# Kernel tuning notes

Measured on AMD Instinct MI355X. Metric: run time of the kernel, lower is better.

## Reference

```python
import jax, jax.numpy as jnp
import numpy as np

B, OUT, EXC_IN, INH_IN, BF = 8192, 1024, 4096, 2048, 4
K_EXC, K_INH = 32, 16


def _pruned_weight(pre_w, K):
    # TopKLinear.pruned_weight: mask of top-K entries (by pre_w) times exp(pre_w)
    w = jnp.exp(pre_w)                      # param_space='log'
    _, idx = jax.lax.top_k(pre_w, K)        # [out, K] indices per row
    rows = jnp.arange(pre_w.shape[0])[:, None]
    mask = jnp.zeros_like(pre_w).at[rows, idx].set(1.0)
    return mask * w


def setup_inputs() -> dict:
    key = jax.random.key(0)
    ks = jax.random.split(key, 5)
    return {
        "x": jax.random.normal(ks[0], (B, EXC_IN), jnp.float32),
        "inhibitory_input": jax.random.normal(ks[1], (B, INH_IN), jnp.float32),
        "branch_input": jax.random.normal(ks[2], (B, OUT * BF), jnp.float32),
        "pre_w_exc": jax.random.uniform(ks[3], (OUT, EXC_IN), jnp.float32, -2.1, -2.0),
        "pre_w_inh": jax.random.uniform(ks[4], (OUT, INH_IN), jnp.float32, -2.1, -2.0),
        "w_block": jnp.ones((OUT, BF), jnp.float32),          # BlockLinear weight (init ones, frozen)
        "presigmoid_Vth": jnp.full((OUT,), -2.0, jnp.float32),  # uniform(-2,-2) == constant
        "log_alpha_max": jnp.zeros((OUT,), jnp.float32),
    }


def reference(x, inhibitory_input, branch_input, pre_w_exc, pre_w_inh,
              w_block, presigmoid_Vth, log_alpha_max):
    # TopKLinear forward: x @ pruned_weight.T
    excitation = x @ _pruned_weight(pre_w_exc, K_EXC).T            # [B, OUT]
    inhibition = inhibitory_input @ _pruned_weight(pre_w_inh, K_INH).T  # [B, OUT]

    # BlockLinear: scatter w_block into block-diagonal [OUT, OUT*BF] then mm;
    # equivalent contraction over the block dim only.
    current = jnp.einsum('nob,ob->no', branch_input.reshape(B, OUT, BF), w_block)
    conductance = jnp.sum(w_block, axis=1)                         # [OUT]

    numerator = excitation + current
    denominator = excitation + 1.0 + conductance + inhibition
    voltage = numerator / denominator

    # reactivation
    Vth = jax.nn.sigmoid(presigmoid_Vth)
    V_diff = voltage - Vth
    rate = jnp.exp(log_alpha_max) * V_diff * V_diff
    return jnp.where(V_diff < 0, jnp.zeros((), voltage.dtype), rate)
```

## Files before the change

### kernel.cpp

```cpp
#include <hip/hip_runtime.h>
#include <cstdint>
#include <cstddef>

#define B_ROWS 8192
#define OUT_N  1024
#define EXC_IN 4096
#define INH_IN 2048
#define K_EXC  32
#define K_INH  16

#define TILE_N       2
#define MAIN_THREADS 1024
#define NBLK         512
#define NT_PER_BLK   (B_ROWS / TILE_N / NBLK)
#define COMB_FLOATS  ((EXC_IN + INH_IN) * TILE_N)
#define CHUNKS       (COMB_FLOATS / 64)
#define CHUNKS_PER_WAVE (CHUNKS / (MAIN_THREADS / 64))
#define XCHUNKS      (EXC_IN * TILE_N / 64)

template<int COLS, int K>
__device__ __forceinline__ void topk_row(const float* __restrict__ src,
                                         float2* __restrict__ ocol, int lane)
{
    constexpr int E4 = COLS / 256;
    unsigned long long keys[E4 * 4];
#pragma unroll
    for (int i = 0; i < E4; ++i) {
        const float4 v = ((const float4*)src)[i * 64 + lane];
        const float vv[4] = {v.x, v.y, v.z, v.w};
#pragma unroll
        for (int q = 0; q < 4; ++q) {
            const int idx = (i * 64 + lane) * 4 + q;
            const unsigned int u = __float_as_uint(vv[q]);
            const unsigned int m = (u >> 31) ? ~u : (u | 0x80000000u);
            keys[i * 4 + q] = ((unsigned long long)m << 12)
                            | (unsigned long long)(4095 - idx);
        }
    }

    unsigned long long win = 0xFFFFFFFFFFFFFFFFull;
#pragma unroll 1
    for (int r = 0; r < K; ++r) {
        unsigned long long best = 0ull;
#pragma unroll
        for (int i = 0; i < E4 * 4; ++i) {
            const unsigned long long k2 = (keys[i] == win) ? 0ull : keys[i];
            keys[i] = k2;
            best = (k2 > best) ? k2 : best;
        }
#pragma unroll
        for (int m = 1; m < 64; m <<= 1) {
            const unsigned long long o = __shfl_xor(best, m, 64);
            best = (o > best) ? o : best;
        }
        win = best;
        if (lane == 0) {
            const unsigned int idx = 4095u - (unsigned int)(win & 0xFFFull);
            const unsigned int mm  = (unsigned int)(win >> 12);
            const unsigned int u   = (mm & 0x80000000u) ? (mm & 0x7FFFFFFFu) : ~mm;
            const float v = __uint_as_float(u);
            ocol[(size_t)r * OUT_N] = make_float2(expf(v), __uint_as_float(idx));
        }
    }
}

__global__ __launch_bounds__(256, 1) void topk_both_kernel(
    const float* __restrict__ pwe, const float* __restrict__ pwi,
    float2* __restrict__ wexcT, float2* __restrict__ winhT)
{
    const int wid  = (blockIdx.x * 256 + threadIdx.x) >> 6;
    const int lane = threadIdx.x & 63;
    if (wid < OUT_N) {
        topk_row<EXC_IN, K_EXC>(pwe + (size_t)wid * EXC_IN, wexcT + wid, lane);
    } else {
        const int r = wid - OUT_N;
        topk_row<INH_IN, K_INH>(pwi + (size_t)r * INH_IN, winhT + r, lane);
    }
}

typedef __attribute__((address_space(1))) const unsigned int gu32_t;
typedef __attribute__((address_space(3))) unsigned int lu32_t;

__global__ __launch_bounds__(MAIN_THREADS, 4) void dendritic_main_kernel(
    const float*  __restrict__ x,
    const float*  __restrict__ inh,
    const float4* __restrict__ branch,
    const float2* __restrict__ wexcT,
    const float2* __restrict__ winhT,
    const float4* __restrict__ wblock,
    const float*  __restrict__ presig,
    const float*  __restrict__ logalpha,
    float*        __restrict__ out)
{
    __shared__ float sx[2][COMB_FLOATS];

    const int tid  = threadIdx.x;
    const int lane = tid & 63;
    const int w    = tid >> 6;
    const int o    = tid;

    const float4 wb   = wblock[o];
    const float cond  = wb.x + wb.y + wb.z + wb.w;
    const float Vth   = 1.f / (1.f + expf(-presig[o]));
    const float alpha = expf(logalpha[o]);

    const int tile0 = blockIdx.x * NT_PER_BLK;
    const int srow  = lane & 1;
    const int scol  = lane >> 1;

    {
        const int n0 = tile0 * TILE_N;
        const float* xs = x   + (size_t)(n0 + srow) * EXC_IN + scol;
        const float* is = inh + (size_t)(n0 + srow) * INH_IN + scol;
#pragma unroll
        for (int i = 0; i < CHUNKS_PER_WAVE; ++i) {
            const int c = i * 16 + w;
            const float* src = (c < XCHUNKS) ? (xs + c * 32)
                                             : (is + (c - XCHUNKS) * 32);
            __builtin_amdgcn_global_load_lds((gu32_t*)src,
                                             (lu32_t*)(&sx[0][0] + c * 64),
                                             4, 0, 0);
        }
    }

#pragma unroll 1
    for (int t = 0; t < NT_PER_BLK; ++t) {
        const int n0 = (tile0 + t) * TILE_N;
        const float* buf = &sx[t & 1][0];

        if (t + 1 < NT_PER_BLK) {
            const int n1 = n0 + TILE_N;
            const float* xs = x   + (size_t)(n1 + srow) * EXC_IN + scol;
            const float* is = inh + (size_t)(n1 + srow) * INH_IN + scol;
            float* dst = &sx[(t + 1) & 1][0];
#pragma unroll
            for (int i = 0; i < CHUNKS_PER_WAVE; ++i) {
                const int c = i * 16 + w;
                const float* src = (c < XCHUNKS) ? (xs + c * 32)
                                                 : (is + (c - XCHUNKS) * 32);
                __builtin_amdgcn_global_load_lds((gu32_t*)src,
                                                 (lu32_t*)(dst + c * 64),
                                                 4, 0, 0);
            }
        }

        const float4 br0 = branch[(size_t)(n0 + 0) * OUT_N + o];
        const float4 br1 = branch[(size_t)(n0 + 1) * OUT_N + o];

        if (t + 1 < NT_PER_BLK) {
            asm volatile("s_waitcnt vmcnt(14)" ::: "memory");
        } else {
            asm volatile("s_waitcnt vmcnt(2)" ::: "memory");
        }
        __builtin_amdgcn_s_barrier();

        float e0 = 0.f, e1 = 0.f;
#pragma unroll 8
        for (int k = 0; k < K_EXC; ++k) {
            const float2 wv = wexcT[k * OUT_N + o];
            const int c = (int)__float_as_uint(wv.y);
            const float2 xv = ((const float2*)buf)[c];
            e0 = fmaf(xv.x, wv.x, e0);
            e1 = fmaf(xv.y, wv.x, e1);
        }

        float i0 = 0.f, i1 = 0.f;
#pragma unroll 8
        for (int k = 0; k < K_INH; ++k) {
            const float2 wv = winhT[k * OUT_N + o];
            const int c = (int)__float_as_uint(wv.y);
            const float2 xv = ((const float2*)buf)[EXC_IN + c];
            i0 = fmaf(xv.x, wv.x, i0);
            i1 = fmaf(xv.y, wv.x, i1);
        }

        {
            const float cur0 = br0.x * wb.x + br0.y * wb.y + br0.z * wb.z + br0.w * wb.w;
            const float cur1 = br1.x * wb.x + br1.y * wb.y + br1.z * wb.z + br1.w * wb.w;
            const float v0 = (e0 + cur0) / (e0 + 1.f + cond + i0);
            const float v1 = (e1 + cur1) / (e1 + 1.f + cond + i1);
            const float d0 = v0 - Vth;
            const float d1 = v1 - Vth;
            const float r0 = alpha * d0 * d0;
            const float r1 = alpha * d1 * d1;
            out[(size_t)(n0 + 0) * OUT_N + o] = (d0 < 0.f) ? 0.f : r0;
            out[(size_t)(n0 + 1) * OUT_N + o] = (d1 < 0.f) ? 0.f : r1;
        }

        __builtin_amdgcn_s_barrier();
    }
}

extern "C" void kernel_launch(void* const* d_in, const int* in_sizes, int n_in,
                              void* d_out, int out_size, void* d_ws, size_t ws_size,
                              hipStream_t stream)
{
    const float* x      = (const float*)d_in[0];
    const float* inh    = (const float*)d_in[1];
    const float* branch = (const float*)d_in[2];
    const float* pwe    = (const float*)d_in[3];
    const float* pwi    = (const float*)d_in[4];
    const float* wb     = (const float*)d_in[5];
    const float* ps     = (const float*)d_in[6];
    const float* la     = (const float*)d_in[7];
    float* out = (float*)d_out;

    float2* wexcT = (float2*)d_ws;
    float2* winhT = (float2*)((char*)d_ws + (size_t)OUT_N * K_EXC * sizeof(float2));

    topk_both_kernel<<<(2 * OUT_N) / 4, 256, 0, stream>>>(pwe, pwi, wexcT, winhT);

    dendritic_main_kernel<<<NBLK, MAIN_THREADS, 0, stream>>>(
        x, inh, (const float4*)branch, wexcT, winhT,
        (const float4*)wb, ps, la, out);
}
```

Measured before the change: 465.7 us.

## Cache top-K weights and packed LDS byte offsets in registers, halve grid

The top-K kernel now writes weights and byte offsets into separate arrays, packing two 16-bit LDS byte offsets per word with the inhibitory base folded in. The main kernel loads all 48 weights and 24 packed offsets into registers once per thread, so the per-tile loop no longer re-reads them from global memory. The grid drops from 512 to 256 blocks so each block processes more tiles and amortises that register preload. The next-tile staging now issues after the branch loads, with the wait counts adjusted to match. The costs are much higher register pressure under 1024-thread blocks, which risks spills, and fewer blocks in flight.

```diff
diff --git a/kernel.cpp b/kernel.cpp
--- a/kernel.cpp
+++ b/kernel.cpp
@@ -11,16 +11,20 @@
 
 #define TILE_N       2
 #define MAIN_THREADS 1024
-#define NBLK         512
+#define NBLK         256
 #define NT_PER_BLK   (B_ROWS / TILE_N / NBLK)
-#define COMB_FLOATS  ((EXC_IN + INH_IN) * TILE_N)
-#define CHUNKS       (COMB_FLOATS / 64)
-#define CHUNKS_PER_WAVE (CHUNKS / (MAIN_THREADS / 64))
+#define BUF_FLOATS   ((EXC_IN + INH_IN) * TILE_N)
+#define BUF_BYTES    (BUF_FLOATS * 4)
+#define CHUNKS       (BUF_FLOATS / 64)
+#define CPW          (CHUNKS / (MAIN_THREADS / 64))
 #define XCHUNKS      (EXC_IN * TILE_N / 64)
+#define INH_BASE_B   (EXC_IN * TILE_N * 4)
 
 template<int COLS, int K>
 __device__ __forceinline__ void topk_row(const float* __restrict__ src,
-                                         float2* __restrict__ ocol, int lane)
+                                         float* __restrict__ vals,
+                                         unsigned int* __restrict__ offs,
+                                         unsigned int bias, int lane)
 {
     constexpr int E4 = COLS / 256;
     unsigned long long keys[E4 * 4];
@@ -39,6 +43,7 @@
     }
 
     unsigned long long win = 0xFFFFFFFFFFFFFFFFull;
+    unsigned int prev = 0;
 #pragma unroll 1
     for (int r = 0; r < K; ++r) {
         unsigned long long best = 0ull;
@@ -59,22 +64,28 @@
             const unsigned int mm  = (unsigned int)(win >> 12);
             const unsigned int u   = (mm & 0x80000000u) ? (mm & 0x7FFFFFFFu) : ~mm;
             const float v = __uint_as_float(u);
-            ocol[(size_t)r * OUT_N] = make_float2(expf(v), __uint_as_float(idx));
+            vals[(size_t)r * OUT_N] = expf(v);
+            const unsigned int bo = idx * 8u + bias;
+            if (r & 1) offs[(size_t)(r >> 1) * OUT_N] = prev | (bo << 16);
+            else       prev = bo;
         }
     }
 }
 
 __global__ __launch_bounds__(256, 1) void topk_both_kernel(
     const float* __restrict__ pwe, const float* __restrict__ pwi,
-    float2* __restrict__ wexcT, float2* __restrict__ winhT)
+    float* __restrict__ valsE, unsigned int* __restrict__ offE,
+    float* __restrict__ valsI, unsigned int* __restrict__ offI)
 {
     const int wid  = (blockIdx.x * 256 + threadIdx.x) >> 6;
     const int lane = threadIdx.x & 63;
     if (wid < OUT_N) {
-        topk_row<EXC_IN, K_EXC>(pwe + (size_t)wid * EXC_IN, wexcT + wid, lane);
+        topk_row<EXC_IN, K_EXC>(pwe + (size_t)wid * EXC_IN,
+                                valsE + wid, offE + wid, 0u, lane);
     } else {
         const int r = wid - OUT_N;
-        topk_row<INH_IN, K_INH>(pwi + (size_t)r * INH_IN, winhT + r, lane);
+        topk_row<INH_IN, K_INH>(pwi + (size_t)r * INH_IN,
+                                valsI + r, offI + r, (unsigned)INH_BASE_B, lane);
     }
 }
 
@@ -85,20 +96,33 @@
     const float*  __restrict__ x,
     const float*  __restrict__ inh,
     const float4* __restrict__ branch,
-    const float2* __restrict__ wexcT,
-    const float2* __restrict__ winhT,
+    const float*  __restrict__ valsE,
+    const unsigned int* __restrict__ offE,
+    const float*  __restrict__ valsI,
+    const unsigned int* __restrict__ offI,
     const float4* __restrict__ wblock,
     const float*  __restrict__ presig,
     const float*  __restrict__ logalpha,
     float*        __restrict__ out)
 {
-    __shared__ float sx[2][COMB_FLOATS];
+    __shared__ float sx[2 * BUF_FLOATS];
 
     const int tid  = threadIdx.x;
     const int lane = tid & 63;
     const int w    = tid >> 6;
     const int o    = tid;
 
+    float vE[K_EXC]; unsigned int oE[K_EXC / 2];
+    float vI[K_INH]; unsigned int oI[K_INH / 2];
+#pragma unroll
+    for (int k = 0; k < K_EXC; ++k)     vE[k] = valsE[(size_t)k * OUT_N + o];
+#pragma unroll
+    for (int k = 0; k < K_EXC / 2; ++k) oE[k] = offE[(size_t)k * OUT_N + o];
+#pragma unroll
+    for (int k = 0; k < K_INH; ++k)     vI[k] = valsI[(size_t)k * OUT_N + o];
+#pragma unroll
+    for (int k = 0; k < K_INH / 2; ++k) oI[k] = offI[(size_t)k * OUT_N + o];
+
     const float4 wb   = wblock[o];
     const float cond  = wb.x + wb.y + wb.z + wb.w;
     const float Vth   = 1.f / (1.f + expf(-presig[o]));
@@ -108,70 +132,64 @@
     const int srow  = lane & 1;
     const int scol  = lane >> 1;
 
-    {
-        const int n0 = tile0 * TILE_N;
-        const float* xs = x   + (size_t)(n0 + srow) * EXC_IN + scol;
-        const float* is = inh + (size_t)(n0 + srow) * INH_IN + scol;
-#pragma unroll
-        for (int i = 0; i < CHUNKS_PER_WAVE; ++i) {
+    auto stage = [&](int tile, int bufidx) {
+        const int n = tile * TILE_N;
+        const float* xs = x   + (size_t)(n + srow) * EXC_IN + scol;
+        const float* is = inh + (size_t)(n + srow) * INH_IN + scol;
+        float* dst = sx + bufidx * BUF_FLOATS;
+#pragma unroll
+        for (int i = 0; i < CPW; ++i) {
             const int c = i * 16 + w;
             const float* src = (c < XCHUNKS) ? (xs + c * 32)
                                              : (is + (c - XCHUNKS) * 32);
             __builtin_amdgcn_global_load_lds((gu32_t*)src,
-                                             (lu32_t*)(&sx[0][0] + c * 64),
-                                             4, 0, 0);
-        }
-    }
+                                             (lu32_t*)(dst + c * 64), 4, 0, 0);
+        }
+    };
+
+    stage(tile0, 0);
 
 #pragma unroll 1
     for (int t = 0; t < NT_PER_BLK; ++t) {
         const int n0 = (tile0 + t) * TILE_N;
-        const float* buf = &sx[t & 1][0];
-
-        if (t + 1 < NT_PER_BLK) {
-            const int n1 = n0 + TILE_N;
-            const float* xs = x   + (size_t)(n1 + srow) * EXC_IN + scol;
-            const float* is = inh + (size_t)(n1 + srow) * INH_IN + scol;
-            float* dst = &sx[(t + 1) & 1][0];
-#pragma unroll
-            for (int i = 0; i < CHUNKS_PER_WAVE; ++i) {
-                const int c = i * 16 + w;
-                const float* src = (c < XCHUNKS) ? (xs + c * 32)
-                                                 : (is + (c - XCHUNKS) * 32);
-                __builtin_amdgcn_global_load_lds((gu32_t*)src,
-                                                 (lu32_t*)(dst + c * 64),
-                                                 4, 0, 0);
-            }
-        }
 
         const float4 br0 = branch[(size_t)(n0 + 0) * OUT_N + o];
         const float4 br1 = branch[(size_t)(n0 + 1) * OUT_N + o];
+
+        if (t + 1 < NT_PER_BLK) stage(tile0 + t + 1, (t + 1) & 1);
 
         if (t + 1 < NT_PER_BLK) {
             asm volatile("s_waitcnt vmcnt(14)" ::: "memory");
         } else {
-            asm volatile("s_waitcnt vmcnt(2)" ::: "memory");
+            asm volatile("s_waitcnt vmcnt(4)" ::: "memory");
         }
         __builtin_amdgcn_s_barrier();
+        __builtin_amdgcn_sched_barrier(0);
+
+        const char* bufb = (const char*)sx + (size_t)(t & 1) * BUF_BYTES;
 
         float e0 = 0.f, e1 = 0.f;
-#pragma unroll 8
-        for (int k = 0; k < K_EXC; ++k) {
-            const float2 wv = wexcT[k * OUT_N + o];
-            const int c = (int)__float_as_uint(wv.y);
-            const float2 xv = ((const float2*)buf)[c];
-            e0 = fmaf(xv.x, wv.x, e0);
-            e1 = fmaf(xv.y, wv.x, e1);
+#pragma unroll
+        for (int k2 = 0; k2 < K_EXC / 2; ++k2) {
+            const unsigned int pw = oE[k2];
+            const float2 a = *(const float2*)(bufb + (pw & 0xFFFFu));
+            const float2 b = *(const float2*)(bufb + (pw >> 16));
+            e0 = fmaf(a.x, vE[2 * k2],     e0);
+            e1 = fmaf(a.y, vE[2 * k2],     e1);
+            e0 = fmaf(b.x, vE[2 * k2 + 1], e0);
+            e1 = fmaf(b.y, vE[2 * k2 + 1], e1);
         }
 
         float i0 = 0.f, i1 = 0.f;
-#pragma unroll 8
-        for (int k = 0; k < K_INH; ++k) {
-            const float2 wv = winhT[k * OUT_N + o];
-            const int c = (int)__float_as_uint(wv.y);
-            const float2 xv = ((const float2*)buf)[EXC_IN + c];
-            i0 = fmaf(xv.x, wv.x, i0);
-            i1 = fmaf(xv.y, wv.x, i1);
+#pragma unroll
+        for (int k2 = 0; k2 < K_INH / 2; ++k2) {
+            const unsigned int pw = oI[k2];
+            const float2 a = *(const float2*)(bufb + (pw & 0xFFFFu));
+            const float2 b = *(const float2*)(bufb + (pw >> 16));
+            i0 = fmaf(a.x, vI[2 * k2],     i0);
+            i1 = fmaf(a.y, vI[2 * k2],     i1);
+            i0 = fmaf(b.x, vI[2 * k2 + 1], i0);
+            i1 = fmaf(b.y, vI[2 * k2 + 1], i1);
         }
 
         {
@@ -205,12 +223,16 @@
     const float* la     = (const float*)d_in[7];
     float* out = (float*)d_out;
 
-    float2* wexcT = (float2*)d_ws;
-    float2* winhT = (float2*)((char*)d_ws + (size_t)OUT_N * K_EXC * sizeof(float2));
-
-    topk_both_kernel<<<(2 * OUT_N) / 4, 256, 0, stream>>>(pwe, pwi, wexcT, winhT);
+    char* ws = (char*)d_ws;
+    float*        valsE = (float*)ws;
+    unsigned int* offE  = (unsigned int*)(ws + 128 * 1024);
+    float*        valsI = (float*)(ws + 192 * 1024);
+    unsigned int* offI  = (unsigned int*)(ws + 256 * 1024);
+
+    topk_both_kernel<<<(2 * OUT_N) / 4, 256, 0, stream>>>(
+        pwe, pwi, valsE, offE, valsI, offI);
 
     dendritic_main_kernel<<<NBLK, MAIN_THREADS, 0, stream>>>(
-        x, inh, (const float4*)branch, wexcT, winhT,
+        x, inh, (const float4*)branch, valsE, offE, valsI, offI,
         (const float4*)wb, ps, la, out);
 }
```

Result: slower. 577.0 us (+23.9%).
